# Kernel optimization log

Measured on AMD Instinct MI355X. Metric: run time of the kernel, lower is better.

Reference implementation:

```python
import jax, jax.numpy as jnp
import numpy as np

GRID_SIZE = 5       # efficient-KAN defaults
SPLINE_ORDER = 3
GRID_RANGE = (-1.0, 1.0)
N_BASIS = GRID_SIZE + SPLINE_ORDER  # 8
LN_EPS = 1e-5


def _make_grid(in_features):
    h = (GRID_RANGE[1] - GRID_RANGE[0]) / GRID_SIZE
    g = np.arange(-SPLINE_ORDER, GRID_SIZE + SPLINE_ORDER + 1, dtype=np.float32) * h + GRID_RANGE[0]
    return jnp.asarray(np.tile(g, (in_features, 1)))  # [in, G+2k+1]


def _b_splines(x, grid):
    # x: [N, in], grid: [in, G+2k+1] -> [N, in, G+k]
    x = x[..., None]
    bases = ((x >= grid[:, :-1]) & (x < grid[:, 1:])).astype(x.dtype)
    for k in range(1, SPLINE_ORDER + 1):
        bases = ((x - grid[:, : -(k + 1)]) / (grid[:, k:-1] - grid[:, : -(k + 1)]) * bases[..., :-1]
                 + (grid[:, k + 1:] - x) / (grid[:, k + 1:] - grid[:, 1:-k]) * bases[..., 1:])
    return bases


def _layer_norm(x, scale, bias):
    mu = jnp.mean(x, axis=-1, keepdims=True)
    var = jnp.mean(jnp.square(x - mu), axis=-1, keepdims=True)
    return (x - mu) * jax.lax.rsqrt(var + LN_EPS) * scale + bias


def setup_inputs() -> dict:
    key = jax.random.key(0)
    B, S, D = 2, 4096, 256
    IN = 3 * D
    ks = jax.random.split(key, 20)
    s = 0.02
    inp = {
        'axial_tokens': jax.random.normal(ks[0], (B, S, D), jnp.float32),
        'sagittal_tokens': jax.random.normal(ks[1], (B, S, D), jnp.float32),
        'coronal_tokens': jax.random.normal(ks[2], (B, S, D), jnp.float32),
        'wq': jax.random.normal(ks[3], (D, D), jnp.float32) * s,
        'bq': jnp.zeros((D,), jnp.float32),
        'wk': jax.random.normal(ks[4], (D, D), jnp.float32) * s,
        'bk': jnp.zeros((D,), jnp.float32),
        'wv': jax.random.normal(ks[5], (D, D), jnp.float32) * s,
        'bv': jnp.zeros((D,), jnp.float32),
        'view_emb': jax.random.normal(ks[6], (3, D), jnp.float32) * s,
        'ln_ax_scale': jnp.ones((D,), jnp.float32), 'ln_ax_bias': jnp.zeros((D,), jnp.float32),
        'ln_sg_scale': jnp.ones((D,), jnp.float32), 'ln_sg_bias': jnp.zeros((D,), jnp.float32),
        'ln_co_scale': jnp.ones((D,), jnp.float32), 'ln_co_bias': jnp.zeros((D,), jnp.float32),
        'base_weight': jax.random.normal(ks[7], (D, IN), jnp.float32) * s,
        'spline_weight': jax.random.normal(ks[8], (D, IN, N_BASIS), jnp.float32) * s,
        'spline_scaler': 1.0 + jax.random.normal(ks[9], (D, IN), jnp.float32) * 0.1,
    }
    return inp


def reference(axial_tokens, sagittal_tokens, coronal_tokens,
              wq, bq, wk, bk, wv, bv, view_emb,
              ln_ax_scale, ln_ax_bias, ln_sg_scale, ln_sg_bias, ln_co_scale, ln_co_bias,
              base_weight, spline_weight, spline_scaler):
    D = axial_tokens.shape[-1]
    inv_sqrt_d = 1.0 / jnp.sqrt(jnp.float32(D))

    def attend(tokens, emb, ln_s, ln_b):
        q = tokens @ wq.T + bq
        k = tokens @ wk.T + bk
        v = tokens @ wv.T + bv
        # torch adds q @ view_emb_row_broadcast^T: every column of the bias equals q . emb
        bias = (q @ emb)[..., None]                      # [B,S,1]
        scores = jnp.einsum('bqd,bkd->bqk', q, k) * inv_sqrt_d + bias
        w = jax.nn.softmax(scores, axis=-1)
        att = jnp.einsum('bqk,bkd->bqd', w, v)
        return _layer_norm(att + tokens, ln_s, ln_b)

    ax = attend(axial_tokens, view_emb[0], ln_ax_scale, ln_ax_bias)
    sg = attend(sagittal_tokens, view_emb[1], ln_sg_scale, ln_sg_bias)
    co = attend(coronal_tokens, view_emb[2], ln_co_scale, ln_co_bias)

    x = jnp.concatenate((ax, sg, co), axis=-1)          # [B,S,3D]
    B, S, IN = x.shape
    grid = _make_grid(IN)
    base = jax.nn.silu(x) @ base_weight.T               # [B,S,D]
    sb = _b_splines(x.reshape(-1, IN), grid)            # [B*S, IN, G+k]
    sw = spline_weight * spline_scaler[..., None]       # [D, IN, G+k]
    spline = jnp.einsum('nif,oif->no', sb, sw).reshape(B, S, -1)
    return base + spline
```

## Files before the change

### kernel.cpp

```cpp
#include <hip/hip_runtime.h>
#include <hip/hip_bf16.h>
#include <math.h>


typedef __hip_bfloat16 bf16;
using bf16x8 = __attribute__((ext_vector_type(8))) __bf16;
using f32x4  = __attribute__((ext_vector_type(4))) float;

__device__ __forceinline__ void load_lds16(const void* g, void* l) {
  __builtin_amdgcn_global_load_lds((__attribute__((address_space(1))) void*)g,
                                   (__attribute__((address_space(3))) void*)l,
                                   16, 0, 0);
}

__device__ __forceinline__ float wave_sum(float v) {
#pragma unroll
  for (int o = 32; o > 0; o >>= 1) v += __shfl_down(v, o, 64);
  return v;
}

__device__ __forceinline__ float b3_cardinal(float x, float tofs) {
  const float t = fmaf(x, 2.5f, tofs);
  const float tc = fminf(fmaxf(t, 0.0f), 4.0f);
  const float p2 = fmaxf(tc - 1.0f, 0.0f);
  const float p3 = fmaxf(tc - 2.0f, 0.0f);
  const float p4 = fmaxf(tc - 3.0f, 0.0f);
  return (tc * tc * tc - 4.0f * p2 * p2 * p2 + 6.0f * p3 * p3 * p3 -
          4.0f * p4 * p4 * p4) * (1.0f / 6.0f);
}

template <typename OutT, bool EXP>
__global__ __launch_bounds__(256) void mfma_gemm_bt(
    const bf16* __restrict__ A, const bf16* __restrict__ B,
    const float* __restrict__ bias, OutT* __restrict__ C,
    float* __restrict__ lpart, int K, int lda, int ldb, int ldc, int zshift,
    size_t zAh, size_t zAl, size_t zBh, size_t zBl, size_t zC, size_t zL,
    float scale) {
  __shared__ __align__(16) bf16 As[4096];
  __shared__ __align__(16) bf16 Bs[4096];
  const int tid = (int)threadIdx.x;
  const int lane = tid & 63;
  const int w = tid >> 6;
  const int m0 = (int)blockIdx.y << 7;
  const int n0 = (int)blockIdx.x << 7;
  const size_t z = blockIdx.z;
  const size_t zlo = z & (((size_t)1 << zshift) - 1);
  A += (z >> zshift) * zAh + zlo * zAl;
  B += (z >> zshift) * zBh + zlo * zBl;
  C += z * zC;
  if (EXP) lpart += z * zL;

  const int srow = lane >> 2;
  const int qg = (lane & 3) ^ ((lane >> 3) & 3);
  const int ci0 = w, ci1 = w + 4;
  const bf16* gA0 = A + (size_t)(m0 + ci0 * 16 + srow) * lda + qg * 8;
  const bf16* gA1 = A + (size_t)(m0 + ci1 * 16 + srow) * lda + qg * 8;
  const bf16* gB0 = B + (size_t)(n0 + ci0 * 16 + srow) * ldb + qg * 8;
  const bf16* gB1 = B + (size_t)(n0 + ci1 * 16 + srow) * ldb + qg * 8;
  bf16* lA0 = As + ci0 * 512;
  bf16* lA1 = As + ci1 * 512;
  bf16* lB0 = Bs + ci0 * 512;
  bf16* lB1 = Bs + ci1 * 512;

  const int m15 = lane & 15, quad = lane >> 4;
  const int fq = quad ^ ((m15 >> 1) & 3);
  const int aoff = m15 * 32 + fq * 8;
  const bf16* pA = As + ((w >> 1) << 11) + aoff;
  const bf16* pB = Bs + ((w & 1) << 11) + aoff;

  f32x4 acc[4][4];
#pragma unroll
  for (int mi = 0; mi < 4; ++mi)
#pragma unroll
    for (int ni = 0; ni < 4; ++ni) acc[mi][ni] = (f32x4)(0.0f);

  for (int k0 = 0; k0 < K; k0 += 32) {
    load_lds16(gA0, lA0);
    load_lds16(gA1, lA1);
    load_lds16(gB0, lB0);
    load_lds16(gB1, lB1);
    gA0 += 32; gA1 += 32; gB0 += 32; gB1 += 32;
    __syncthreads();
    bf16x8 av[4], bv[4];
#pragma unroll
    for (int i = 0; i < 4; ++i) {
      av[i] = *(const bf16x8*)(pA + i * 512);
      bv[i] = *(const bf16x8*)(pB + i * 512);
    }
#pragma unroll
    for (int mi = 0; mi < 4; ++mi)
#pragma unroll
      for (int ni = 0; ni < 4; ++ni)
        acc[mi][ni] = __builtin_amdgcn_mfma_f32_16x16x32_bf16(
            av[mi], bv[ni], acc[mi][ni], 0, 0, 0);
    __syncthreads();
  }

  const int crow = m0 + ((w >> 1) << 6) + quad * 4;
  const int ccol = n0 + ((w & 1) << 6) + m15;
  float rs[4][4] = {};
#pragma unroll
  for (int ni = 0; ni < 4; ++ni) {
    const int col = ccol + ni * 16;
    const float bb = bias ? bias[col] : 0.0f;
#pragma unroll
    for (int mi = 0; mi < 4; ++mi) {
#pragma unroll
      for (int i = 0; i < 4; ++i) {
        const int row = crow + mi * 16 + i;
        float v = acc[mi][ni][i] * scale + bb;
        if constexpr (EXP) {
          v = __expf(v);
          rs[mi][i] += v;
        }
        if constexpr (sizeof(OutT) == 2)
          C[(size_t)row * ldc + col] = __float2bfloat16(v);
        else
          C[(size_t)row * ldc + col] = v;
      }
    }
  }
  if constexpr (EXP) {
    const int ch = ((int)blockIdx.x << 1) | (w & 1);
#pragma unroll
    for (int mi = 0; mi < 4; ++mi)
#pragma unroll
      for (int i = 0; i < 4; ++i) {
        float sv = rs[mi][i];
        sv += __shfl_xor(sv, 1);
        sv += __shfl_xor(sv, 2);
        sv += __shfl_xor(sv, 4);
        sv += __shfl_xor(sv, 8);
        if (m15 == 0)
          lpart[(size_t)ch * 4096 + crow + mi * 16 + i] = sv;
      }
  }
}

template <bool FUSE>
__global__ __launch_bounds__(256) void resid_ln_kernel(
    const float* __restrict__ attp, const float* __restrict__ lpart,
    const float* __restrict__ tok, const float* __restrict__ gamma,
    const float* __restrict__ beta, float* __restrict__ xout,
    bf16* __restrict__ basis, int vIdx) {
  __shared__ float red[4];
  __shared__ float sinvl;
  __shared__ __align__(16) bf16 st[2304];
  const int n = (int)blockIdx.x;
  const int d = (int)threadIdx.x;
  const int b = n >> 12, r = n & 4095;
  float ls = 0.f;
  if (d < 64) ls = lpart[((size_t)(b * 64 + d)) * 4096 + r];
  ls = wave_sum(ls);
  if (d == 0) sinvl = 1.0f / ls;
  const size_t abase = (size_t)(b * 4) * 1048576 + (size_t)r * 256 + d;
  const float asum = attp[abase] + attp[abase + 1048576] +
                     attp[abase + 2097152] + attp[abase + 3145728];
  __syncthreads();
  const float y = asum * sinvl + tok[(size_t)n * 256 + d];
  float s = wave_sum(y);
  if ((d & 63) == 0) red[d >> 6] = s;
  __syncthreads();
  const float mu = (red[0] + red[1] + red[2] + red[3]) * (1.0f / 256.0f);
  __syncthreads();
  const float c = y - mu;
  float s2 = wave_sum(c * c);
  if ((d & 63) == 0) red[d >> 6] = s2;
  __syncthreads();
  const float var = (red[0] + red[1] + red[2] + red[3]) * (1.0f / 256.0f);
  const float rstd = rsqrtf(var + 1e-5f);
  const float val = c * rstd * gamma[d] + beta[d];
  if constexpr (!FUSE) {
    xout[(size_t)n * 768 + vIdx * 256 + d] = val;
  } else {
#pragma unroll
    for (int f = 0; f < 8; ++f)
      st[d * 9 + f] = __float2bfloat16(b3_cardinal(val, 5.5f - (float)f));
    st[d * 9 + 8] = __float2bfloat16(val / (1.0f + __expf(-val)));
    __syncthreads();
    float4* gb = (float4*)((char*)basis + (size_t)n * 13824 + vIdx * 4608);
    const float4* sb = (const float4*)st;
    gb[d] = sb[d];
    if (d < 32) gb[256 + d] = sb[256 + d];
  }
}

__global__ __launch_bounds__(256) void prep_w(
    const float* __restrict__ bw, const float* __restrict__ sw,
    const float* __restrict__ scaler, bf16* __restrict__ Wmat) {
  const int o = blockIdx.x;
  for (int ii = 0; ii < 3; ++ii) {
    const int i = ii * 256 + (int)threadIdx.x;
    const float s = scaler[(size_t)o * 768 + i];
    bf16* p = Wmat + (size_t)o * 6912 + i * 9;
    const float* swp = sw + ((size_t)o * 768 + i) * 8;
#pragma unroll
    for (int f = 0; f < 8; ++f) p[f] = __float2bfloat16(swp[f] * s);
    p[8] = __float2bfloat16(bw[(size_t)o * 768 + i]);
  }
}

__global__ __launch_bounds__(256) void prep_qkvw(
    const float* __restrict__ wq, const float* __restrict__ wk,
    const float* __restrict__ wv, const float* __restrict__ bq,
    const float* __restrict__ bk, const float* __restrict__ bv,
    bf16* __restrict__ wqkvb, float* __restrict__ bqkv) {
  const int idx = blockIdx.x * 256 + (int)threadIdx.x;
  const int row = idx >> 8, col = idx & 255;
  const float* src = row < 256 ? wq : (row < 512 ? wk : wv);
  wqkvb[idx] = __float2bfloat16(src[((row & 255) << 8) + col]);
  if (idx < 768)
    bqkv[idx] = idx < 256 ? bq[idx] : (idx < 512 ? bk[idx - 256] : bv[idx - 512]);
}

__global__ __launch_bounds__(256) void cast_tok3(
    const float4* __restrict__ t0, const float4* __restrict__ t1,
    const float4* __restrict__ t2, bf16* __restrict__ dst) {
  const int vv = blockIdx.y;
  const float4* src = vv == 0 ? t0 : (vv == 1 ? t1 : t2);
  const int idx = blockIdx.x * 256 + (int)threadIdx.x;
  const float4 val = src[idx];
  bf16* p = dst + (size_t)vv * 2097152 + (size_t)idx * 4;
  p[0] = __float2bfloat16(val.x);
  p[1] = __float2bfloat16(val.y);
  p[2] = __float2bfloat16(val.z);
  p[3] = __float2bfloat16(val.w);
}

__global__ __launch_bounds__(256) void transpose_v(
    const bf16* __restrict__ qkv, bf16* __restrict__ vT) {
  __shared__ bf16 tle[64][65];
  const int s0 = blockIdx.x << 6, d0 = blockIdx.y << 6, z = blockIdx.z;
  const int tid = (int)threadIdx.x;
  const int c = tid & 63, rr = tid >> 6;
  for (int r = 0; r < 64; r += 4)
    tle[r + rr][c] = qkv[(size_t)(z * 4096 + s0 + r + rr) * 768 + 512 + d0 + c];
  __syncthreads();
  for (int r = 0; r < 64; r += 4)
    vT[(size_t)z * 1048576 + (size_t)(d0 + r + rr) * 4096 + s0 + c] =
        tle[c][r + rr];
}

__global__ __launch_bounds__(256) void basis_kernel(
    const float* __restrict__ x, bf16* __restrict__ basis) {
  const int i = blockIdx.x * 256 + (int)threadIdx.x;
  const int n = blockIdx.y;
  const float xv = x[(size_t)n * 768 + i];
  float b[11];
#pragma unroll
  for (int m = 0; m < 11; ++m) {
    const float g0 = 0.4f * (float)(m - 3) - 1.0f;
    const float g1 = 0.4f * (float)(m - 2) - 1.0f;
    b[m] = (xv >= g0 && xv < g1) ? 1.0f : 0.0f;
  }
#pragma unroll
  for (int k = 1; k <= 3; ++k) {
    const float inv = 1.0f / (0.4f * (float)k);
#pragma unroll
    for (int m = 0; m + k < 11; ++m) {
      const float gm = 0.4f * (float)(m - 3) - 1.0f;
      const float gmk1 = 0.4f * (float)(m + k - 2) - 1.0f;
      b[m] = (xv - gm) * inv * b[m] + (gmk1 - xv) * inv * b[m + 1];
    }
  }
  bf16* p = basis + (size_t)n * 6912 + i * 9;
#pragma unroll
  for (int f = 0; f < 8; ++f) p[f] = __float2bfloat16(b[f]);
  p[8] = __float2bfloat16(xv / (1.0f + __expf(-xv)));
}

__global__ __launch_bounds__(256) void combine4_kernel(
    const float4* __restrict__ p, float4* __restrict__ out) {
  const int idx = blockIdx.x * 256 + (int)threadIdx.x;
  const float4 a = p[idx];
  const float4 b = p[idx + 524288];
  const float4 c = p[idx + 1048576];
  const float4 d = p[idx + 1572864];
  out[idx] =
      make_float4(a.x + b.x + c.x + d.x, a.y + b.y + c.y + d.y,
                  a.z + b.z + c.z + d.z, a.w + b.w + c.w + d.w);
}

extern "C" void kernel_launch(void* const* d_in, const int* in_sizes, int n_in,
                              void* d_out, int out_size, void* d_ws,
                              size_t ws_size, hipStream_t stream) {
  const float* tok[3] = {(const float*)d_in[0], (const float*)d_in[1],
                         (const float*)d_in[2]};
  const float* wq = (const float*)d_in[3];
  const float* bq = (const float*)d_in[4];
  const float* wk = (const float*)d_in[5];
  const float* bk = (const float*)d_in[6];
  const float* wv = (const float*)d_in[7];
  const float* bv = (const float*)d_in[8];
  const float* lng[3] = {(const float*)d_in[10], (const float*)d_in[12],
                         (const float*)d_in[14]};
  const float* lnb[3] = {(const float*)d_in[11], (const float*)d_in[13],
                         (const float*)d_in[15]};
  const float* bw = (const float*)d_in[16];
  const float* sw = (const float*)d_in[17];
  const float* scaler = (const float*)d_in[18];

  const bool fused = ws_size >= 282856448ull;
  char* w8 = (char*)d_ws;
  bf16* tokb = (bf16*)(w8 + 0);
  bf16* qkv = (bf16*)(w8 + 12582912);
  bf16* vT = (bf16*)(w8 + 50331648);
  bf16* Pb = (bf16*)(w8 + 62914560);
  float* lpart = (float*)(w8 + 130023424);
  float* attp = (float*)(w8 + 132120576);
  float* pout = attp;
  float* x;
  bf16* basis;
  bf16* Wmat;
  if (fused) {
    x = nullptr;
    basis = (bf16*)(w8 + 165675008);
    Wmat = (bf16*)(w8 + 278921216);
  } else {
    x = (float*)(w8 + 165675008);
    basis = (bf16*)(w8 + 0);
    Wmat = (bf16*)(w8 + 190840832);
  }
  bf16* wqkvb = (bf16*)((char*)Wmat + 3538944);
  float* bqkv = (float*)((char*)wqkvb + 393216);

  prep_w<<<256, 256, 0, stream>>>(bw, sw, scaler, Wmat);
  prep_qkvw<<<768, 256, 0, stream>>>(wq, wk, wv, bq, bk, bv, wqkvb, bqkv);
  cast_tok3<<<dim3(2048, 3), 256, 0, stream>>>(
      (const float4*)tok[0], (const float4*)tok[1], (const float4*)tok[2],
      tokb);

  mfma_gemm_bt<bf16, false><<<dim3(6, 192, 1), 256, 0, stream>>>(
      tokb, wqkvb, bqkv, qkv, nullptr, 256, 256, 256, 768, 1, 0, 0, 0, 0, 0,
      0, 1.0f);
  transpose_v<<<dim3(64, 4, 6), 256, 0, stream>>>(qkv, vT);

  for (int v = 0; v < 3; ++v) {
    const bf16* qb = qkv + (size_t)(2 * v) * 4096 * 768;
    mfma_gemm_bt<bf16, true><<<dim3(32, 32, 2), 256, 0, stream>>>(
        qb, qb + 256, nullptr, Pb, lpart, 256, 768, 768, 4096, 1, 0, 3145728,
        0, 3145728, 16777216, 262144, 0.0625f);
    mfma_gemm_bt<float, false><<<dim3(2, 32, 8), 256, 0, stream>>>(
        Pb, vT + (size_t)(2 * v) * 1048576, nullptr, attp, nullptr, 1024,
        4096, 4096, 256, 2, 16777216, 1024, 1048576, 1024, 1048576, 0, 1.0f);
    if (fused)
      resid_ln_kernel<true><<<8192, 256, 0, stream>>>(
          attp, lpart, tok[v], lng[v], lnb[v], nullptr, basis, v);
    else
      resid_ln_kernel<false><<<8192, 256, 0, stream>>>(
          attp, lpart, tok[v], lng[v], lnb[v], x, nullptr, v);
  }

  if (!fused) basis_kernel<<<dim3(3, 8192), 256, 0, stream>>>(x, basis);

  mfma_gemm_bt<float, false><<<dim3(2, 64, 4), 256, 0, stream>>>(
      basis, Wmat, nullptr, pout, nullptr, 1728, 6912, 6912, 256, 2, 0, 1728,
      0, 1728, 2097152, 0, 1.0f);
  combine4_kernel<<<2048, 256, 0, stream>>>((const float4*)pout,
                                            (float4*)d_out);
}
```

Before: 528.7 us.

## Double GEMM K-tile to 64 and split final KAN GEMM six ways

```diff
diff --git a/kernel.cpp b/kernel.cpp
--- a/kernel.cpp
+++ b/kernel.cpp
@@ -36,8 +36,8 @@
     float* __restrict__ lpart, int K, int lda, int ldb, int ldc, int zshift,
     size_t zAh, size_t zAl, size_t zBh, size_t zBl, size_t zC, size_t zL,
     float scale) {
-  __shared__ __align__(16) bf16 As[4096];
-  __shared__ __align__(16) bf16 Bs[4096];
+  __shared__ __align__(16) bf16 As[8192];
+  __shared__ __align__(16) bf16 Bs[8192];
   const int tid = (int)threadIdx.x;
   const int lane = tid & 63;
   const int w = tid >> 6;
@@ -50,23 +50,25 @@
   C += z * zC;
   if (EXP) lpart += z * zL;
 
-  const int srow = lane >> 2;
-  const int qg = (lane & 3) ^ ((lane >> 3) & 3);
-  const int ci0 = w, ci1 = w + 4;
-  const bf16* gA0 = A + (size_t)(m0 + ci0 * 16 + srow) * lda + qg * 8;
-  const bf16* gA1 = A + (size_t)(m0 + ci1 * 16 + srow) * lda + qg * 8;
-  const bf16* gB0 = B + (size_t)(n0 + ci0 * 16 + srow) * ldb + qg * 8;
-  const bf16* gB1 = B + (size_t)(n0 + ci1 * 16 + srow) * ldb + qg * 8;
-  bf16* lA0 = As + ci0 * 512;
-  bf16* lA1 = As + ci1 * 512;
-  bf16* lB0 = Bs + ci0 * 512;
-  bf16* lB1 = Bs + ci1 * 512;
+  const int srow8 = lane >> 3;
+  const int g8 = (lane & 4) | ((lane & 3) ^ ((lane >> 4) & 3));
+  const bf16* gA[4];
+  const bf16* gB[4];
+  bf16* lA[4];
+  bf16* lB[4];
+#pragma unroll
+  for (int j = 0; j < 4; ++j) {
+    const int c = w + 4 * j;
+    gA[j] = A + (size_t)(m0 + c * 8 + srow8) * lda + g8 * 8;
+    gB[j] = B + (size_t)(n0 + c * 8 + srow8) * ldb + g8 * 8;
+    lA[j] = As + c * 512;
+    lB[j] = Bs + c * 512;
+  }
 
   const int m15 = lane & 15, quad = lane >> 4;
   const int fq = quad ^ ((m15 >> 1) & 3);
-  const int aoff = m15 * 32 + fq * 8;
-  const bf16* pA = As + ((w >> 1) << 11) + aoff;
-  const bf16* pB = Bs + ((w & 1) << 11) + aoff;
+  const bf16* pA = As + (size_t)(((w >> 1) << 6) + m15) * 64 + fq * 8;
+  const bf16* pB = Bs + (size_t)(((w & 1) << 6) + m15) * 64 + fq * 8;
 
   f32x4 acc[4][4];
 #pragma unroll
@@ -74,25 +76,31 @@
 #pragma unroll
     for (int ni = 0; ni < 4; ++ni) acc[mi][ni] = (f32x4)(0.0f);
 
-  for (int k0 = 0; k0 < K; k0 += 32) {
-    load_lds16(gA0, lA0);
-    load_lds16(gA1, lA1);
-    load_lds16(gB0, lB0);
-    load_lds16(gB1, lB1);
-    gA0 += 32; gA1 += 32; gB0 += 32; gB1 += 32;
+  for (int k0 = 0; k0 < K; k0 += 64) {
+#pragma unroll
+    for (int j = 0; j < 4; ++j) {
+      load_lds16(gA[j], lA[j]);
+      load_lds16(gB[j], lB[j]);
+      gA[j] += 64;
+      gB[j] += 64;
+    }
     __syncthreads();
-    bf16x8 av[4], bv[4];
-#pragma unroll
-    for (int i = 0; i < 4; ++i) {
-      av[i] = *(const bf16x8*)(pA + i * 512);
-      bv[i] = *(const bf16x8*)(pB + i * 512);
-    }
+    bf16x8 av[4][2], bv[4][2];
 #pragma unroll
     for (int mi = 0; mi < 4; ++mi)
 #pragma unroll
-      for (int ni = 0; ni < 4; ++ni)
-        acc[mi][ni] = __builtin_amdgcn_mfma_f32_16x16x32_bf16(
-            av[mi], bv[ni], acc[mi][ni], 0, 0, 0);
+      for (int sub = 0; sub < 2; ++sub) {
+        av[mi][sub] = *(const bf16x8*)(pA + mi * 1024 + sub * 32);
+        bv[mi][sub] = *(const bf16x8*)(pB + mi * 1024 + sub * 32);
+      }
+#pragma unroll
+    for (int sub = 0; sub < 2; ++sub)
+#pragma unroll
+      for (int mi = 0; mi < 4; ++mi)
+#pragma unroll
+        for (int ni = 0; ni < 4; ++ni)
+          acc[mi][ni] = __builtin_amdgcn_mfma_f32_16x16x32_bf16(
+              av[mi][sub], bv[ni][sub], acc[mi][ni], 0, 0, 0);
     __syncthreads();
   }
 
@@ -281,6 +289,21 @@
                   a.z + b.z + c.z + d.z, a.w + b.w + c.w + d.w);
 }
 
+__global__ __launch_bounds__(256) void combine6_kernel(
+    const float4* __restrict__ p, float4* __restrict__ out) {
+  const int idx = blockIdx.x * 256 + (int)threadIdx.x;
+  float4 s = p[idx];
+#pragma unroll
+  for (int j = 1; j < 6; ++j) {
+    const float4 a = p[idx + (size_t)j * 524288];
+    s.x += a.x;
+    s.y += a.y;
+    s.z += a.z;
+    s.w += a.w;
+  }
+  out[idx] = s;
+}
+
 extern "C" void kernel_launch(void* const* d_in, const int* in_sizes, int n_in,
                               void* d_out, int out_size, void* d_ws,
                               size_t ws_size, hipStream_t stream) {
@@ -308,18 +331,20 @@
   bf16* Pb = (bf16*)(w8 + 62914560);
   float* lpart = (float*)(w8 + 130023424);
   float* attp = (float*)(w8 + 132120576);
-  float* pout = attp;
   float* x;
   bf16* basis;
   bf16* Wmat;
+  float* pout;
   if (fused) {
     x = nullptr;
     basis = (bf16*)(w8 + 165675008);
     Wmat = (bf16*)(w8 + 278921216);
+    pout = (float*)Pb;
   } else {
     x = (float*)(w8 + 165675008);
     basis = (bf16*)(w8 + 0);
     Wmat = (bf16*)(w8 + 190840832);
+    pout = attp;
   }
   bf16* wqkvb = (bf16*)((char*)Wmat + 3538944);
   float* bqkv = (float*)((char*)wqkvb + 393216);
@@ -351,11 +376,18 @@
           attp, lpart, tok[v], lng[v], lnb[v], x, nullptr, v);
   }
 
-  if (!fused) basis_kernel<<<dim3(3, 8192), 256, 0, stream>>>(x, basis);
-
-  mfma_gemm_bt<float, false><<<dim3(2, 64, 4), 256, 0, stream>>>(
-      basis, Wmat, nullptr, pout, nullptr, 1728, 6912, 6912, 256, 2, 0, 1728,
-      0, 1728, 2097152, 0, 1.0f);
-  combine4_kernel<<<2048, 256, 0, stream>>>((const float4*)pout,
-                                            (float4*)d_out);
-}
+  if (fused) {
+    mfma_gemm_bt<float, false><<<dim3(2, 64, 6), 256, 0, stream>>>(
+        basis, Wmat, nullptr, pout, nullptr, 1152, 6912, 6912, 256, 3, 0,
+        1152, 0, 1152, 2097152, 0, 1.0f);
+    combine6_kernel<<<2048, 256, 0, stream>>>((const float4*)pout,
+                                              (float4*)d_out);
+  } else {
+    basis_kernel<<<dim3(3, 8192), 256, 0, stream>>>(x, basis);
+    mfma_gemm_bt<float, false><<<dim3(2, 64, 4), 256, 0, stream>>>(
+        basis, Wmat, nullptr, pout, nullptr, 1728, 6912, 6912, 256, 2, 0,
+        1728, 0, 1728, 2097152, 0, 1.0f);
+    combine4_kernel<<<2048, 256, 0, stream>>>((const float4*)pout,
+                                              (float4*)d_out);
+  }
+}
```

Result: faster. 492.1 us (-6.9%).
